# Kernel optimization log

Hardware: AMD Instinct MI355X
Metric: run time of the kernel (lower is better)

## Reference

```python
import jax, jax.numpy as jnp
import numpy as np

B, H, I = 4096, 128, 128


def setup_inputs() -> dict:
    key = jax.random.key(0)
    ks = jax.random.split(key, 9)
    # xavier_uniform for W1/W2: fan_in = 2H*2I, fan_out = H*2I (torch treats dim0 as fan_out for >2D differently,
    # but we only need a plausible init; exact init values don't affect correctness of the math)
    def xavier(k, shape):
        fan_in = shape[1] * shape[2] if len(shape) == 3 else shape[0]
        fan_out = shape[0] * shape[2] if len(shape) == 3 else shape[1]
        lim = np.sqrt(6.0 / (fan_in + fan_out))
        return jax.random.uniform(k, shape, jnp.float32, -lim, lim)
    W1 = xavier(ks[0], (H, 2 * H, 2 * I))
    W2 = xavier(ks[1], (H, 2 * H, 2 * I))
    W3 = xavier(ks[2], (2 * H, H))
    fan_in, fan_out = 2 * H * 2 * I, H * 2 * I
    lim = float(np.sqrt(3.0 / (0.5 * (fan_in + fan_out))))
    b1 = jax.random.uniform(ks[3], (H,), jnp.float32, -lim, lim)
    b2 = jax.random.uniform(ks[4], (H,), jnp.float32, -lim, lim)
    in0 = jax.random.normal(ks[5], (B, I), jnp.float32)
    in1 = jax.random.normal(ks[6], (B, I), jnp.float32)
    st0 = jax.random.normal(ks[7], (B, H), jnp.float32)
    st1 = jax.random.normal(ks[8], (B, H), jnp.float32)
    return {"in0": in0, "in1": in1, "st0": st0, "st1": st1,
            "W1": W1, "b1": b1, "W2": W2, "b2": b2, "W3": W3}


def reference(in0, in1, st0, st1, W1, b1, W2, b2, W3):
    s = jnp.concatenate([st0, st1], axis=1)  # [B, 2H]
    x = jnp.concatenate([in0, in1], axis=1)  # [B, 2I]
    # Trilinear contraction; same math as outer-product-then-contract:
    # einsum('ij,ik->ijk') then ('ijk,ljk->il')  ==  'bj,bk,ljk->bl'
    m1 = jnp.einsum('bj,bk,ljk->bl', s, x, W1)  # [B, H]
    m2 = jnp.einsum('bj,bk,ljk->bl', s, x, W2)  # [B, H]
    u = jax.nn.sigmoid(m2 + b2)
    state_tilda = jnp.tanh(m1 + b1)
    new_state = u * state_tilda + (1.0 - u) * (s @ W3)
    return new_state
```

## Files before the change

kernel.cpp:

```cpp
#include <hip/hip_runtime.h>
#include <hip/hip_bf16.h>
#include <stdint.h>


typedef short bf8 __attribute__((ext_vector_type(8)));
typedef float f32x4 __attribute__((ext_vector_type(4)));

static constexpr size_t WT_OFF  = 0;
static constexpr size_t XBF_OFF = 33554432 + 2097152;
static constexpr size_t MP_OFF  = XBF_OFF + 2097152;

__device__ __forceinline__ unsigned f2bf(float f) {
    unsigned u = __builtin_bit_cast(unsigned, f);
    return (u + 0x7fffu + ((u >> 16) & 1u)) >> 16;
}
__device__ __forceinline__ unsigned pack2bf(float a, float b) {
    return f2bf(a) | (f2bf(b) << 16);
}

__global__ void prep_wx(const float* __restrict__ W1, const float* __restrict__ W2,
                        const float* __restrict__ in0, const float* __restrict__ in1,
                        uint4* __restrict__ Wt, unsigned* __restrict__ x_bf) {
    int bx = blockIdx.x;
    if (bx < 8192) {
        const int tid  = threadIdx.x;
        const int lane = tid & 63, wave = tid >> 6;
        const unsigned f = bx * 4 + wave;
        const unsigned n16 = f >> 11;
        const unsigned kchunk = (f >> 1) & 1023u;
        const unsigned kst = f & 1u;
        const unsigned n = n16 * 16 + (lane & 15);
        const unsigned K = kchunk * 64 + kst * 32 + (lane >> 4) * 8;
        const float* src = (n < 128 ? W1 + ((size_t)n << 16)
                                    : W2 + ((size_t)(n - 128) << 16)) + K;
        float4 a = ((const float4*)src)[0];
        float4 b = ((const float4*)src)[1];
        uint4 o;
        o.x = pack2bf(a.x, a.y); o.y = pack2bf(a.z, a.w);
        o.z = pack2bf(b.x, b.y); o.w = pack2bf(b.z, b.w);
        Wt[(size_t)f * 64 + lane] = o;
    } else {
        unsigned v = (bx - 8192) * 256 + threadIdx.x;
        unsigned b = v >> 6;
        unsigned j4 = (v & 63u) * 4u;
        const float* src = (j4 < 128) ? (in0 + (size_t)b * 128 + j4)
                                      : (in1 + (size_t)b * 128 + (j4 - 128));
        float4 a = *(const float4*)src;
        uint2 o;
        o.x = pack2bf(a.x, a.y);
        o.y = pack2bf(a.z, a.w);
        ((uint2*)x_bf)[v] = o;
    }
}

__launch_bounds__(256, 2)
__global__ void gemm_p(const unsigned char* __restrict__ Wt,
                       const float* __restrict__ st0, const float* __restrict__ st1,
                       const __hip_bfloat16* __restrict__ x_bf,
                       float* __restrict__ Mpart) {
    const int bx = blockIdx.x;
    const int ks = bx & 7;
    const int ntq = (bx >> 3) & 3;
    const int mt = bx >> 5;
    const int b0 = mt << 7, n0 = ntq << 6;
    const int tid  = threadIdx.x;
    const int lane = tid & 63, wave = tid >> 6;
    const int l15 = lane & 15, l4 = lane >> 4;

    __shared__ __align__(16) float Sl[32 * 132];
    for (int idx = tid; idx < 4096; idx += 256) {
        int r = idx >> 5, j = idx & 31;
        int jg = ks * 32 + j;
        float v = (jg < 128) ? st0[(size_t)(b0 + r) * 128 + jg]
                             : st1[(size_t)(b0 + r) * 128 + (jg - 128)];
        Sl[j * 132 + r] = v;
    }
    __syncthreads();

    const unsigned char* rb = Wt + ((size_t)(ntq * 4 + wave) << 21) + lane * 16;
    const float* sB = Sl + l4 * 4;

    f32x4 racc[8];
    #pragma unroll
    for (int mf = 0; mf < 8; ++mf)
        racc[mf] = (f32x4){0.f, 0.f, 0.f, 0.f};
    const f32x4 zacc = (f32x4){0.f, 0.f, 0.f, 0.f};

    auto kof = [&](int c) { return (size_t)(((ks * 32 + (c & 31)) * 4 + (c >> 5)) * 2048); };

    bf8 buf[2][2];
    #pragma unroll
    for (int kst = 0; kst < 2; ++kst)
        buf[0][kst] = *(const bf8*)(rb + kof(0) + kst * 1024);

    bf8 a[8][2];

    #pragma unroll 2
    for (int c = 0; c < 128; ++c) {
        const int pp = c & 1;
        const int q = c >> 5, j = c & 31;
        if (j == 0) {
            const __hip_bfloat16* xb = x_bf + q * 64 + l4 * 8;
            #pragma unroll
            for (int mf = 0; mf < 8; ++mf)
                #pragma unroll
                for (int kst = 0; kst < 2; ++kst)
                    a[mf][kst] = *(const bf8*)(xb + (size_t)(b0 + mf * 16 + l15) * 256 + kst * 32);
        }
        {
            const size_t k1 = kof((c + 1) & 127);
            #pragma unroll
            for (int kst = 0; kst < 2; ++kst)
                buf[pp ^ 1][kst] = *(const bf8*)(rb + k1 + kst * 1024);
        }
        f32x4 sv[8];
        #pragma unroll
        for (int mf = 0; mf < 8; ++mf)
            sv[mf] = *(const f32x4*)(sB + j * 132 + mf * 16);
        bf8 bf0 = buf[pp][0];
        bf8 bf1 = buf[pp][1];
        #pragma unroll
        for (int mf = 0; mf < 8; ++mf) {
            f32x4 m0 = __builtin_amdgcn_mfma_f32_16x16x32_bf16(a[mf][0], bf0, zacc, 0, 0, 0);
            m0 = __builtin_amdgcn_mfma_f32_16x16x32_bf16(a[mf][1], bf1, m0, 0, 0, 0);
            racc[mf] += sv[mf] * m0;
        }
    }

    float* mp = Mpart + ((size_t)ks << 20);
    const int nn = n0 + wave * 16 + l15;
    #pragma unroll
    for (int mf = 0; mf < 8; ++mf) {
        int b = b0 + mf * 16 + l4 * 4;
        #pragma unroll
        for (int r = 0; r < 4; ++r)
            mp[(size_t)(b + r) * 256 + nn] = racc[mf][r];
    }
}

__global__ void epilogue(const float* __restrict__ st0, const float* __restrict__ st1,
                         const float* __restrict__ b1, const float* __restrict__ b2,
                         const float* __restrict__ W3, const float* __restrict__ Mpart,
                         float* __restrict__ out) {
    const int tid = threadIdx.x;
    const int h = tid & 127, rg = tid >> 7;
    const int bbase = blockIdx.x * 8;
    __shared__ float srow[8][256];
    #pragma unroll
    for (int i = 0; i < 8; ++i) {
        int idx = i * 256 + tid;
        int r = idx >> 8, j = idx & 255;
        float v = (j < 128) ? st0[(size_t)(bbase + r) * 128 + j]
                            : st1[(size_t)(bbase + r) * 128 + (j - 128)];
        srow[r][j] = v;
    }
    __syncthreads();
    float acc0 = 0.f, acc1 = 0.f, acc2 = 0.f, acc3 = 0.f;
    for (int j = 0; j < 256; ++j) {
        float w = W3[j * 128 + h];
        acc0 += srow[rg][j] * w;
        acc1 += srow[rg + 2][j] * w;
        acc2 += srow[rg + 4][j] * w;
        acc3 += srow[rg + 6][j] * w;
    }
    float accs[4] = {acc0, acc1, acc2, acc3};
    float bb1 = b1[h], bb2 = b2[h];
    #pragma unroll
    for (int i = 0; i < 4; ++i) {
        int b = bbase + rg + i * 2;
        float m1 = 0.f, m2 = 0.f;
        #pragma unroll
        for (int k = 0; k < 8; ++k) {
            m1 += Mpart[((size_t)k << 20) + (size_t)b * 256 + h];
            m2 += Mpart[((size_t)k << 20) + (size_t)b * 256 + 128 + h];
        }
        float u = 1.0f / (1.0f + expf(-(m2 + bb2)));
        float t = tanhf(m1 + bb1);
        out[(size_t)b * 128 + h] = u * t + (1.0f - u) * accs[i];
    }
}

extern "C" void kernel_launch(void* const* d_in, const int* in_sizes, int n_in,
                              void* d_out, int out_size, void* d_ws, size_t ws_size,
                              hipStream_t stream) {
    const float* in0 = (const float*)d_in[0];
    const float* in1 = (const float*)d_in[1];
    const float* st0 = (const float*)d_in[2];
    const float* st1 = (const float*)d_in[3];
    const float* W1  = (const float*)d_in[4];
    const float* b1  = (const float*)d_in[5];
    const float* W2  = (const float*)d_in[6];
    const float* b2  = (const float*)d_in[7];
    const float* W3  = (const float*)d_in[8];
    float* out = (float*)d_out;
    char* ws = (char*)d_ws;

    unsigned char* Wt   = (unsigned char*)(ws + WT_OFF);
    unsigned*      x_bf = (unsigned*)(ws + XBF_OFF);
    float*         Mp   = (float*)(ws + MP_OFF);

    prep_wx<<<9216, 256, 0, stream>>>(W1, W2, in0, in1, (uint4*)Wt, x_bf);
    gemm_p<<<1024, 256, 0, stream>>>(Wt, st0, st1, (const __hip_bfloat16*)x_bf, Mp);
    epilogue<<<512, 256, 0, stream>>>(st0, st1, b1, b2, W3, Mp, out);
}
```

Before: 285.0 us.

## Pre-transpose state into global buffer, halve GEMM M-tile and double grid

The prep kernel gains extra blocks that transpose the concatenated state into a j-major global buffer. The GEMM kernel then streams state scale factors from that buffer, double-buffered in registers, instead of staging them in LDS behind a barrier. The batch tile per block drops from 128 to 64 rows, so the grid doubles to 2048 blocks and accumulator and register pressure fall. In exchange, each weight tile is reloaded by twice as many blocks, and the state loads now come from global memory rather than LDS.

```diff
diff --git a/kernel.cpp b/kernel.cpp
--- a/kernel.cpp
+++ b/kernel.cpp
@@ -9,6 +9,7 @@
 static constexpr size_t WT_OFF  = 0;
 static constexpr size_t XBF_OFF = 33554432 + 2097152;
 static constexpr size_t MP_OFF  = XBF_OFF + 2097152;
+static constexpr size_t SP_OFF  = MP_OFF + 33554432;
 
 __device__ __forceinline__ unsigned f2bf(float f) {
     unsigned u = __builtin_bit_cast(unsigned, f);
@@ -20,7 +21,9 @@
 
 __global__ void prep_wx(const float* __restrict__ W1, const float* __restrict__ W2,
                         const float* __restrict__ in0, const float* __restrict__ in1,
-                        uint4* __restrict__ Wt, unsigned* __restrict__ x_bf) {
+                        const float* __restrict__ st0, const float* __restrict__ st1,
+                        uint4* __restrict__ Wt, unsigned* __restrict__ x_bf,
+                        float* __restrict__ Sperm) {
     int bx = blockIdx.x;
     if (bx < 8192) {
         const int tid  = threadIdx.x;
@@ -39,7 +42,7 @@
         o.x = pack2bf(a.x, a.y); o.y = pack2bf(a.z, a.w);
         o.z = pack2bf(b.x, b.y); o.w = pack2bf(b.z, b.w);
         Wt[(size_t)f * 64 + lane] = o;
-    } else {
+    } else if (bx < 9216) {
         unsigned v = (bx - 8192) * 256 + threadIdx.x;
         unsigned b = v >> 6;
         unsigned j4 = (v & 63u) * 4u;
@@ -50,50 +53,79 @@
         o.x = pack2bf(a.x, a.y);
         o.y = pack2bf(a.z, a.w);
         ((uint2*)x_bf)[v] = o;
+    } else {
+        const int blk = bx - 9216;
+        const int b0t = (blk >> 2) * 64;
+        const int j0 = (blk & 3) * 64;
+        const int t = threadIdx.x;
+        __shared__ float Lt[64][65];
+        {
+            int r = t >> 2, c4 = (t & 3) * 16;
+            const float* srow = (j0 < 128) ? st0 + (size_t)(b0t + r) * 128 + j0
+                                           : st1 + (size_t)(b0t + r) * 128 + (j0 - 128);
+            #pragma unroll
+            for (int i = 0; i < 4; ++i) {
+                float4 v = *(const float4*)(srow + c4 + i * 4);
+                Lt[r][c4 + i * 4 + 0] = v.x;
+                Lt[r][c4 + i * 4 + 1] = v.y;
+                Lt[r][c4 + i * 4 + 2] = v.z;
+                Lt[r][c4 + i * 4 + 3] = v.w;
+            }
+        }
+        __syncthreads();
+        {
+            int bq = t & 15;
+            #pragma unroll
+            for (int jj = 0; jj < 4; ++jj) {
+                int j = (t >> 4) + jj * 16;
+                float4 o;
+                o.x = Lt[bq * 4 + 0][j];
+                o.y = Lt[bq * 4 + 1][j];
+                o.z = Lt[bq * 4 + 2][j];
+                o.w = Lt[bq * 4 + 3][j];
+                *(float4*)(Sperm + (size_t)(j0 + j) * 4096 + b0t + bq * 4) = o;
+            }
+        }
     }
 }
 
 __launch_bounds__(256, 2)
 __global__ void gemm_p(const unsigned char* __restrict__ Wt,
-                       const float* __restrict__ st0, const float* __restrict__ st1,
+                       const float* __restrict__ Sperm,
                        const __hip_bfloat16* __restrict__ x_bf,
                        float* __restrict__ Mpart) {
     const int bx = blockIdx.x;
     const int ks = bx & 7;
-    const int ntq = (bx >> 3) & 3;
-    const int mt = bx >> 5;
-    const int b0 = mt << 7, n0 = ntq << 6;
+    const int rem = bx >> 3;
+    const int mt = rem & 63;
+    const int ntq = rem >> 6;
+    const int b0 = mt << 6;
     const int tid  = threadIdx.x;
     const int lane = tid & 63, wave = tid >> 6;
     const int l15 = lane & 15, l4 = lane >> 4;
 
-    __shared__ __align__(16) float Sl[32 * 132];
-    for (int idx = tid; idx < 4096; idx += 256) {
-        int r = idx >> 5, j = idx & 31;
-        int jg = ks * 32 + j;
-        float v = (jg < 128) ? st0[(size_t)(b0 + r) * 128 + jg]
-                             : st1[(size_t)(b0 + r) * 128 + (jg - 128)];
-        Sl[j * 132 + r] = v;
-    }
-    __syncthreads();
-
-    const unsigned char* rb = Wt + ((size_t)(ntq * 4 + wave) << 21) + lane * 16;
-    const float* sB = Sl + l4 * 4;
-
-    f32x4 racc[8];
-    #pragma unroll
-    for (int mf = 0; mf < 8; ++mf)
+    const int n16 = ntq * 4 + wave;
+    const unsigned char* rb = Wt + ((size_t)n16 << 21) + lane * 16;
+    const float* sp = Sperm + ((size_t)(ks * 32) << 12) + b0 + l4 * 4;
+
+    f32x4 racc[4];
+    #pragma unroll
+    for (int mf = 0; mf < 4; ++mf)
         racc[mf] = (f32x4){0.f, 0.f, 0.f, 0.f};
     const f32x4 zacc = (f32x4){0.f, 0.f, 0.f, 0.f};
 
     auto kof = [&](int c) { return (size_t)(((ks * 32 + (c & 31)) * 4 + (c >> 5)) * 2048); };
 
     bf8 buf[2][2];
+    f32x4 svb[2][4];
     #pragma unroll
     for (int kst = 0; kst < 2; ++kst)
         buf[0][kst] = *(const bf8*)(rb + kof(0) + kst * 1024);
-
-    bf8 a[8][2];
+    #pragma unroll
+    for (int mf = 0; mf < 4; ++mf)
+        svb[0][mf] = *(const f32x4*)(sp + mf * 16);
+
+    bf8 a[4][2];
 
     #pragma unroll 2
     for (int c = 0; c < 128; ++c) {
@@ -102,35 +134,36 @@
         if (j == 0) {
             const __hip_bfloat16* xb = x_bf + q * 64 + l4 * 8;
             #pragma unroll
-            for (int mf = 0; mf < 8; ++mf)
+            for (int mf = 0; mf < 4; ++mf)
                 #pragma unroll
                 for (int kst = 0; kst < 2; ++kst)
                     a[mf][kst] = *(const bf8*)(xb + (size_t)(b0 + mf * 16 + l15) * 256 + kst * 32);
         }
         {
-            const size_t k1 = kof((c + 1) & 127);
+            const int c1 = (c + 1) & 127;
+            const size_t k1 = kof(c1);
             #pragma unroll
             for (int kst = 0; kst < 2; ++kst)
                 buf[pp ^ 1][kst] = *(const bf8*)(rb + k1 + kst * 1024);
-        }
-        f32x4 sv[8];
-        #pragma unroll
-        for (int mf = 0; mf < 8; ++mf)
-            sv[mf] = *(const f32x4*)(sB + j * 132 + mf * 16);
+            const int j1 = c1 & 31;
+            #pragma unroll
+            for (int mf = 0; mf < 4; ++mf)
+                svb[pp ^ 1][mf] = *(const f32x4*)(sp + ((size_t)j1 << 12) + mf * 16);
+        }
         bf8 bf0 = buf[pp][0];
         bf8 bf1 = buf[pp][1];
         #pragma unroll
-        for (int mf = 0; mf < 8; ++mf) {
+        for (int mf = 0; mf < 4; ++mf) {
             f32x4 m0 = __builtin_amdgcn_mfma_f32_16x16x32_bf16(a[mf][0], bf0, zacc, 0, 0, 0);
             m0 = __builtin_amdgcn_mfma_f32_16x16x32_bf16(a[mf][1], bf1, m0, 0, 0, 0);
-            racc[mf] += sv[mf] * m0;
+            racc[mf] += svb[pp][mf] * m0;
         }
     }
 
     float* mp = Mpart + ((size_t)ks << 20);
-    const int nn = n0 + wave * 16 + l15;
-    #pragma unroll
-    for (int mf = 0; mf < 8; ++mf) {
+    const int nn = n16 * 16 + l15;
+    #pragma unroll
+    for (int mf = 0; mf < 4; ++mf) {
         int b = b0 + mf * 16 + l4 * 4;
         #pragma unroll
         for (int r = 0; r < 4; ++r)
@@ -198,8 +231,10 @@
     unsigned char* Wt   = (unsigned char*)(ws + WT_OFF);
     unsigned*      x_bf = (unsigned*)(ws + XBF_OFF);
     float*         Mp   = (float*)(ws + MP_OFF);
-
-    prep_wx<<<9216, 256, 0, stream>>>(W1, W2, in0, in1, (uint4*)Wt, x_bf);
-    gemm_p<<<1024, 256, 0, stream>>>(Wt, st0, st1, (const __hip_bfloat16*)x_bf, Mp);
+    float*         Sp   = (float*)(ws + SP_OFF);
+
+    prep_wx<<<9472, 256, 0, stream>>>(W1, W2, in0, in1, st0, st1,
+                                      (uint4*)Wt, x_bf, Sp);
+    gemm_p<<<2048, 256, 0, stream>>>(Wt, Sp, (const __hip_bfloat16*)x_bf, Mp);
     epilogue<<<512, 256, 0, stream>>>(st0, st1, b1, b2, W3, Mp, out);
 }
```

Result: slower. 346.1 us (+21.4%).
